# Kernel tuning notes

Measured on AMD Instinct MI355X. Metric: run time of the kernel, lower is better.

The kernel has to match this reference:

```python
import jax, jax.numpy as jnp
import numpy as np

B, S, D, H = 2, 2048, 1024, 16
DK = D // H
NEG = -1.0e9

def setup_inputs() -> dict:
    key = jax.random.key(0)
    ks = jax.random.split(key, 12)
    sc = 1.0 / np.sqrt(D)
    q = jax.random.normal(ks[0], (B, S, D), jnp.float32)
    k = jax.random.normal(ks[1], (B, S, D), jnp.float32)
    v = jax.random.normal(ks[2], (B, S, D), jnp.float32)
    # causal mask: True = masked (matches masked_fill(mask == True, -1e9))
    mask = jnp.broadcast_to(jnp.triu(jnp.ones((S, S), bool), k=1)[None, None], (B, 1, S, S))
    Wq = jax.random.normal(ks[3], (D, D), jnp.float32) * sc
    bq = jnp.zeros((D,), jnp.float32)
    Wk = jax.random.normal(ks[4], (D, D), jnp.float32) * sc
    bk = jnp.zeros((D,), jnp.float32)
    Wv = jax.random.normal(ks[5], (D, D), jnp.float32) * sc
    bv = jnp.zeros((D,), jnp.float32)
    Wo = jax.random.normal(ks[6], (D, D), jnp.float32) * sc
    bo = jnp.zeros((D,), jnp.float32)
    return {"q": q, "k": k, "v": v, "mask": mask,
            "Wq": Wq, "bq": bq, "Wk": Wk, "bk": bk,
            "Wv": Wv, "bv": bv, "Wo": Wo, "bo": bo}

def reference(q, k, v, mask, Wq, bq, Wk, bk, Wv, bv, Wo, bo):
    def split_heads(x):  # [B,S,D] -> [B,H,S,DK]
        return x.reshape(B, S, H, DK).transpose(0, 2, 1, 3)
    qh = split_heads(q @ Wq + bq)
    kh = split_heads(k @ Wk + bk)
    vh = split_heads(v @ Wv + bv)
    scores = jnp.einsum('bhqd,bhkd->bhqk', qh, kh) / np.sqrt(DK)
    scores = jnp.where(mask, NEG, scores)
    p = jax.nn.softmax(scores, axis=-1)
    out = jnp.einsum('bhqk,bhkd->bhqd', p, vh)  # [B,H,S,DK]
    out = out.transpose(0, 2, 1, 3).reshape(B, S, D)
    return out @ Wo + bo
```

## Files before the change

kernel.cpp:

```cpp
#include <hip/hip_runtime.h>

#define BB 2
#define SS 2048
#define DD 1024
#define HH 16
#define DKK 64

typedef __attribute__((ext_vector_type(8))) short short8;
typedef __attribute__((ext_vector_type(4))) float floatx4;

__device__ inline float bf2f(ushort u) {
    union { unsigned int i; float f; } x; x.i = ((unsigned int)u) << 16; return x.f;
}
__device__ inline ushort f2bf(float f) {
    union { float f; unsigned int i; } x; x.f = f;
    unsigned int r = x.i + 0x7fff + ((x.i >> 16) & 1);
    return (ushort)(r >> 16);
}
__device__ inline void async_cp16(const ushort* g, ushort* l) {
    __builtin_amdgcn_global_load_lds(
        (const __attribute__((address_space(1))) unsigned int*)g,
        (__attribute__((address_space(3))) unsigned int*)l, 16, 0, 0);
}
__device__ inline unsigned int cvt_pk_bf16(float lo, float hi) {
    unsigned int r;
    asm("v_cvt_pk_bf16_f32 %0, %1, %2" : "=v"(r) : "v"(lo), "v"(hi));
    return r;
}
__device__ inline void swap32(unsigned int& a, unsigned int& b) {
    asm("v_permlane32_swap_b32 %0, %1" : "+v"(a), "+v"(b));
}
__device__ inline void swap16(unsigned int& a, unsigned int& b) {
    asm("v_permlane16_swap_b32 %0, %1" : "+v"(a), "+v"(b));
}

__global__ __launch_bounds__(256) void cvt_w4(const float* __restrict__ w0,
                                              const float* __restrict__ w1,
                                              const float* __restrict__ w2,
                                              const float* __restrict__ w3,
                                              ushort* __restrict__ o0,
                                              ushort* __restrict__ o1,
                                              ushort* __restrict__ o2,
                                              ushort* __restrict__ o3) {
    __shared__ ushort t[32][33];
    int z = blockIdx.z;
    const float* in = (z == 0) ? w0 : (z == 1) ? w1 : (z == 2) ? w2 : w3;
    ushort* out = (z == 0) ? o0 : (z == 1) ? o1 : (z == 2) ? o2 : o3;
    int bx = blockIdx.x, by = blockIdx.y, tx = threadIdx.x;
    for (int i = threadIdx.y; i < 32; i += 8)
        t[i][tx] = f2bf(in[(size_t)(by * 32 + i) * DD + bx * 32 + tx]);
    __syncthreads();
    for (int i = threadIdx.y; i < 32; i += 8)
        out[(size_t)(bx * 32 + i) * DD + by * 32 + tx] = t[tx][i];
}

__global__ __launch_bounds__(256) void cvt_qkv(const float* __restrict__ q,
                                               const float* __restrict__ k,
                                               const float* __restrict__ v,
                                               ushort* __restrict__ oq,
                                               ushort* __restrict__ ok,
                                               ushort* __restrict__ ov) {
    int z = blockIdx.z;
    const float* in = (z == 0) ? q : (z == 1) ? k : v;
    ushort* out = (z == 0) ? oq : (z == 1) ? ok : ov;
    int i = blockIdx.x * 256 + threadIdx.x;
    float4 f0 = ((const float4*)in)[i * 2];
    float4 f1 = ((const float4*)in)[i * 2 + 1];
    short8 p;
    p[0] = (short)f2bf(f0.x); p[1] = (short)f2bf(f0.y);
    p[2] = (short)f2bf(f0.z); p[3] = (short)f2bf(f0.w);
    p[4] = (short)f2bf(f1.x); p[5] = (short)f2bf(f1.y);
    p[6] = (short)f2bf(f1.z); p[7] = (short)f2bf(f1.w);
    ((short8*)out)[i] = p;
}

__global__ __launch_bounds__(512, 2) void gemm_qkv(const ushort* __restrict__ Xq,
                                                   const ushort* __restrict__ Xk,
                                                   const ushort* __restrict__ Xv,
                                                   const ushort* __restrict__ WtQ,
                                                   const ushort* __restrict__ WtK,
                                                   const ushort* __restrict__ WtV,
                                                   const float* __restrict__ bq,
                                                   const float* __restrict__ bk,
                                                   const float* __restrict__ bv,
                                                   ushort* __restrict__ qh,
                                                   ushort* __restrict__ kh,
                                                   ushort* __restrict__ vt) {
    constexpr int K = 1024;
    constexpr int NKT = 32;
    __shared__ ushort smem[32768];

    int lin = blockIdx.x + (blockIdx.y << 2) + (blockIdx.z << 6);
    int wid = (lin & 7) * 24 + (lin >> 3);
    int z = wid >> 6;
    int rem = wid & 63;
    int byy = rem >> 2, bxx = rem & 3;
    int rowBase = byy * 256, colBase = bxx * 256;

    const ushort* Ag = (z == 0) ? Xq : (z == 1) ? Xk : Xv;
    const ushort* Bg = (z == 0) ? WtQ : (z == 1) ? WtK : WtV;
    const float* bias = (z == 0) ? bq : (z == 1) ? bk : bv;
    ushort* outp = (z == 0) ? qh : (z == 1) ? kh : vt;

    int tid = threadIdx.x;
    int wave = tid >> 6, lane = tid & 63, quad = lane >> 4, l15 = lane & 15;
    int wm = wave >> 2, wn = wave & 3;

    size_t srcA[2], srcB[2];
    int dstU[2];
#pragma unroll
    for (int r = 0; r < 2; ++r) {
        int lb = r * 8192 + wave * 1024 + lane * 16;
        int sl = lb ^ (((lb >> 9) & 1) << 5);
        int srow = sl >> 6;
        int scol = (sl & 63) >> 1;
        srcA[r] = (size_t)(rowBase + srow) * K + scol;
        srcB[r] = (size_t)(colBase + srow) * K + scol;
        dstU[r] = r * 4096 + wave * 512;
    }
    int aOff[2][4], bOff[4];
#pragma unroll
    for (int mh = 0; mh < 2; ++mh)
#pragma unroll
        for (int mi = 0; mi < 4; ++mi) {
            int row = wm * 128 + mh * 64 + mi * 16 + l15;
            aOff[mh][mi] = row * 32 + ((quad * 8) ^ (((row >> 3) & 1) << 4));
        }
#pragma unroll
    for (int ni = 0; ni < 4; ++ni) {
        int row = wn * 64 + ni * 16 + l15;
        bOff[ni] = 8192 + row * 32 + ((quad * 8) ^ (((row >> 3) & 1) << 4));
    }

    auto stageTile = [&](int u) {
        int slot = (u & 1) << 14;
        const ushort* As = Ag + u * 32;
        const ushort* Bs = Bg + u * 32;
        async_cp16(As + srcA[0], &smem[slot + dstU[0]]);
        async_cp16(As + srcA[1], &smem[slot + dstU[1]]);
        async_cp16(Bs + srcB[0], &smem[slot + 8192 + dstU[0]]);
        async_cp16(Bs + srcB[1], &smem[slot + 8192 + dstU[1]]);
    };

    floatx4 acc[8][4] = {};
    stageTile(0);
    for (int t = 0; t < NKT; ++t) {
        if (t < NKT - 1) {
            stageTile(t + 1);
            asm volatile("s_waitcnt vmcnt(4)" ::: "memory");
        } else {
            asm volatile("s_waitcnt vmcnt(0)" ::: "memory");
        }
        __builtin_amdgcn_s_barrier();
        __builtin_amdgcn_sched_barrier(0);
        int slot = (t & 1) << 14;
        short8 bfr[4];
#pragma unroll
        for (int ni = 0; ni < 4; ++ni)
            bfr[ni] = *(const short8*)&smem[slot + bOff[ni]];
#pragma unroll
        for (int mh = 0; mh < 2; ++mh) {
            short8 af[4];
#pragma unroll
            for (int mi = 0; mi < 4; ++mi)
                af[mi] = *(const short8*)&smem[slot + aOff[mh][mi]];
#pragma unroll
            for (int mi = 0; mi < 4; ++mi)
#pragma unroll
                for (int ni = 0; ni < 4; ++ni)
                    acc[mh * 4 + mi][ni] = __builtin_amdgcn_mfma_f32_16x16x32_bf16(
                        af[mi], bfr[ni], acc[mh * 4 + mi][ni], 0, 0, 0);
        }
        __builtin_amdgcn_sched_barrier(0);
        __builtin_amdgcn_s_barrier();
    }

    float bvv[4];
#pragma unroll
    for (int ni = 0; ni < 4; ++ni)
        bvv[ni] = bias[colBase + wn * 64 + ni * 16 + l15];
    if (z == 2) {
#pragma unroll
        for (int mi = 0; mi < 8; ++mi)
#pragma unroll
            for (int ni = 0; ni < 4; ++ni) {
                int col = colBase + wn * 64 + ni * 16 + l15;
                int h = col >> 6, dk = col & 63;
                int rowg = rowBase + wm * 128 + mi * 16 + quad * 4;
                int b = rowg >> 11, s = rowg & 2047;
                int2 v;
                v.x = (int)cvt_pk_bf16(acc[mi][ni][0] + bvv[ni], acc[mi][ni][1] + bvv[ni]);
                v.y = (int)cvt_pk_bf16(acc[mi][ni][2] + bvv[ni], acc[mi][ni][3] + bvv[ni]);
                *(int2*)&outp[((size_t)((b * HH + h) * DKK + dk)) * SS + s] = v;
            }
    } else {
#pragma unroll
        for (int mi = 0; mi < 8; ++mi)
#pragma unroll
            for (int ni = 0; ni < 4; ++ni) {
                int col = colBase + wn * 64 + ni * 16 + l15;
                int h = col >> 6, dk = col & 63;
#pragma unroll
                for (int i = 0; i < 4; ++i) {
                    int rowg = rowBase + wm * 128 + mi * 16 + quad * 4 + i;
                    int b = rowg >> 11, s = rowg & 2047;
                    outp[((size_t)((b * HH + h) * SS + s)) * DKK + dk] =
                        f2bf(acc[mi][ni][i] + bvv[ni]);
                }
            }
    }
}

__global__ __launch_bounds__(256) void gemm_fin(const ushort* __restrict__ A,
                                                const ushort* __restrict__ Bt,
                                                const float* __restrict__ bias,
                                                float* __restrict__ outp) {
    constexpr int K = 1024, N = 1024, NT = 32;
    __shared__ ushort smem[12288];
    int tid = threadIdx.x;
    int wave = tid >> 6, lane = tid & 63, quad = lane >> 4, l15 = lane & 15;
    int wm = wave >> 1, wn = wave & 1;

    int lin = blockIdx.x + (blockIdx.y << 3);
    int wid = (lin & 7) * 64 + (lin >> 3);
    int bx = wid & 7, by = wid >> 3;
    int rowBase = by * 64, colBase = bx * 128;

    auto stage = [&](int k0, int d) {
        int ab = d * 6144, bb2 = 2048 + d * 6144;
#pragma unroll
        for (int j = 0; j < 3; ++j) {
            int c = j * 4 + wave;
            int cbase = (c < 4) ? c * 64 : (c - 4) * 64;
            int cc = cbase + lane;
            int row = cc >> 2, sub = (cc & 3) * 8;
            if (c < 4)
                async_cp16(&A[(size_t)(rowBase + row) * K + k0 + sub], &smem[ab + cbase * 8]);
            else
                async_cp16(&Bt[(size_t)(colBase + row) * K + k0 + sub], &smem[bb2 + cbase * 8]);
        }
    };

    floatx4 acc[2][4] = {};
    stage(0, 0);
    __syncthreads();
    for (int t = 0; t < NT; ++t) {
        if (t + 1 < NT) stage((t + 1) * 32, (t + 1) & 1);
        int ab = (t & 1) * 6144, bb2 = 2048 + (t & 1) * 6144;
        short8 af[2], bf[4];
#pragma unroll
        for (int mi = 0; mi < 2; ++mi)
            af[mi] = *(const short8*)&smem[ab + (wm * 32 + mi * 16 + l15) * 32 + quad * 8];
#pragma unroll
        for (int ni = 0; ni < 4; ++ni)
            bf[ni] = *(const short8*)&smem[bb2 + (wn * 64 + ni * 16 + l15) * 32 + quad * 8];
#pragma unroll
        for (int mi = 0; mi < 2; ++mi)
#pragma unroll
            for (int ni = 0; ni < 4; ++ni)
                acc[mi][ni] = __builtin_amdgcn_mfma_f32_16x16x32_bf16(
                    af[mi], bf[ni], acc[mi][ni], 0, 0, 0);
        __syncthreads();
    }
    for (int mi = 0; mi < 2; ++mi)
        for (int ni = 0; ni < 4; ++ni) {
            int col = colBase + wn * 64 + ni * 16 + l15;
            float bv = bias[col];
            for (int i = 0; i < 4; ++i) {
                int row = rowBase + wm * 32 + mi * 16 + quad * 4 + i;
                outp[(size_t)row * N + col] = acc[mi][ni][i] + bv;
            }
        }
}

__global__ __launch_bounds__(256, 2) void flash_attn5(const ushort* __restrict__ qh,
                                                      const ushort* __restrict__ kh,
                                                      const ushort* __restrict__ vt,
                                                      ushort* __restrict__ attn) {
    constexpr int LD = 72;
    __shared__ ushort Ksm[2][64 * LD];
    __shared__ ushort Vsm[2][64 * LD];
    int tid = threadIdx.x;
    int h = blockIdx.y, b = blockIdx.z;
    int wave = tid >> 6, lane = tid & 63, quad = lane >> 4, l15 = lane & 15;
    const size_t headQK = ((size_t)(b * HH + h)) * SS * DKK;
    const size_t headV  = ((size_t)(b * HH + h)) * DKK * SS;
    int c0 = tid, r0 = c0 >> 3, s0 = (c0 & 7) * 8;
    int c1 = tid + 256, r1 = c1 >> 3, s1 = (c1 & 7) * 8;
    const int qt0 = blockIdx.x;
    const int qt1 = 31 - qt0;

    int qrow0 = qt0 * 64 + wave * 16 + l15;
    int qrow1 = qt1 * 64 + wave * 16 + l15;
    short8 q0a = *(const short8*)&qh[headQK + (size_t)qrow0 * DKK + quad * 8];
    short8 q0b = *(const short8*)&qh[headQK + (size_t)qrow0 * DKK + 32 + quad * 8];
    short8 q1a = *(const short8*)&qh[headQK + (size_t)qrow1 * DKK + quad * 8];
    short8 q1b = *(const short8*)&qh[headQK + (size_t)qrow1 * DKK + 32 + quad * 8];

    floatx4 o0[4] = {}, o1[4] = {};
    float l0 = 0.f, l1 = 0.f;
    int qsel = wave * 16 + l15;

    *(int4*)&Ksm[0][r0 * LD + s0] = *(const int4*)&kh[headQK + (size_t)r0 * DKK + s0];
    *(int4*)&Ksm[0][r1 * LD + s1] = *(const int4*)&kh[headQK + (size_t)r1 * DKK + s1];
    *(int4*)&Vsm[0][r0 * LD + s0] = *(const int4*)&vt[headV + (size_t)r0 * SS + s0];
    *(int4*)&Vsm[0][r1 * LD + s1] = *(const int4*)&vt[headV + (size_t)r1 * SS + s1];
    __syncthreads();

    for (int kt = 0; kt <= qt1; ++kt) {
        int cur = kt & 1;
        bool pre = (kt < qt1);
        bool act0 = (kt <= qt0);
        int4 kA, kB, vA, vB;
        if (pre) {
            const ushort* kp = &kh[headQK + (size_t)((kt + 1) * 64) * DKK];
            const ushort* vp = &vt[headV + (kt + 1) * 64];
            kA = *(const int4*)&kp[(size_t)r0 * DKK + s0];
            kB = *(const int4*)&kp[(size_t)r1 * DKK + s1];
            vA = *(const int4*)&vp[(size_t)r0 * SS + s0];
            vB = *(const int4*)&vp[(size_t)r1 * SS + s1];
        }
        floatx4 sv1[4], sv0[4];
#pragma unroll
        for (int cn = 0; cn < 4; ++cn) {
            short8 kf0 = *(const short8*)&Ksm[cur][(cn * 16 + l15) * LD + quad * 8];
            short8 kf1 = *(const short8*)&Ksm[cur][(cn * 16 + l15) * LD + 32 + quad * 8];
            floatx4 zz = {};
            zz = __builtin_amdgcn_mfma_f32_16x16x32_bf16(kf0, q1a, zz, 0, 0, 0);
            zz = __builtin_amdgcn_mfma_f32_16x16x32_bf16(kf1, q1b, zz, 0, 0, 0);
            sv1[cn] = zz;
            if (act0) {
                floatx4 y = {};
                y = __builtin_amdgcn_mfma_f32_16x16x32_bf16(kf0, q0a, y, 0, 0, 0);
                y = __builtin_amdgcn_mfma_f32_16x16x32_bf16(kf1, q0b, y, 0, 0, 0);
                sv0[cn] = y;
            }
        }
        short8 vf[2][4];
#pragma unroll
        for (int ks = 0; ks < 2; ++ks)
#pragma unroll
            for (int n = 0; n < 4; ++n)
                vf[ks][n] = *(const short8*)&Vsm[cur][(n * 16 + l15) * LD + ks * 32 + quad * 8];

        {
            bool diag = (kt == qt1);
            unsigned int pkd[4][2];
#pragma unroll
            for (int cn = 0; cn < 4; ++cn) {
#pragma unroll
                for (int i = 0; i < 4; ++i) {
                    float p = __expf(sv1[cn][i] * 0.125f);
                    if (diag && (cn * 16 + quad * 4 + i) > qsel) p = 0.f;
                    sv1[cn][i] = p;
                    l1 += p;
                }
                pkd[cn][0] = cvt_pk_bf16(sv1[cn][0], sv1[cn][1]);
                pkd[cn][1] = cvt_pk_bf16(sv1[cn][2], sv1[cn][3]);
            }
#pragma unroll
            for (int ks = 0; ks < 2; ++ks) {
                unsigned int a0 = pkd[ks * 2][0], b0 = pkd[ks * 2 + 1][0];
                swap32(a0, b0); swap16(a0, b0);
                unsigned int a1 = pkd[ks * 2][1], b1 = pkd[ks * 2 + 1][1];
                swap32(a1, b1); swap16(a1, b1);
                union { int4 i4; short8 s8; } u;
                u.i4 = make_int4((int)a0, (int)a1, (int)b0, (int)b1);
#pragma unroll
                for (int n = 0; n < 4; ++n)
                    o1[n] = __builtin_amdgcn_mfma_f32_16x16x32_bf16(
                        vf[ks][n], u.s8, o1[n], 0, 0, 0);
            }
        }
        if (act0) {
            bool diag = (kt == qt0);
            unsigned int pkd[4][2];
#pragma unroll
            for (int cn = 0; cn < 4; ++cn) {
#pragma unroll
                for (int i = 0; i < 4; ++i) {
                    float p = __expf(sv0[cn][i] * 0.125f);
                    if (diag && (cn * 16 + quad * 4 + i) > qsel) p = 0.f;
                    sv0[cn][i] = p;
                    l0 += p;
                }
                pkd[cn][0] = cvt_pk_bf16(sv0[cn][0], sv0[cn][1]);
                pkd[cn][1] = cvt_pk_bf16(sv0[cn][2], sv0[cn][3]);
            }
#pragma unroll
            for (int ks = 0; ks < 2; ++ks) {
                unsigned int a0 = pkd[ks * 2][0], b0 = pkd[ks * 2 + 1][0];
                swap32(a0, b0); swap16(a0, b0);
                unsigned int a1 = pkd[ks * 2][1], b1 = pkd[ks * 2 + 1][1];
                swap32(a1, b1); swap16(a1, b1);
                union { int4 i4; short8 s8; } u;
                u.i4 = make_int4((int)a0, (int)a1, (int)b0, (int)b1);
#pragma unroll
                for (int n = 0; n < 4; ++n)
                    o0[n] = __builtin_amdgcn_mfma_f32_16x16x32_bf16(
                        vf[ks][n], u.s8, o0[n], 0, 0, 0);
            }
        }
        if (pre) {
            int nb = cur ^ 1;
            *(int4*)&Ksm[nb][r0 * LD + s0] = kA;
            *(int4*)&Ksm[nb][r1 * LD + s1] = kB;
            *(int4*)&Vsm[nb][r0 * LD + s0] = vA;
            *(int4*)&Vsm[nb][r1 * LD + s1] = vB;
        }
        __syncthreads();
    }
    l0 += __shfl_xor(l0, 16, 64); l0 += __shfl_xor(l0, 32, 64);
    l1 += __shfl_xor(l1, 16, 64); l1 += __shfl_xor(l1, 32, 64);
    float inv0 = 1.0f / l0, inv1 = 1.0f / l1;
    size_t rowOff0 = ((size_t)(b * SS + qt0 * 64 + wave * 16 + l15)) * DD + h * 64;
    size_t rowOff1 = ((size_t)(b * SS + qt1 * 64 + wave * 16 + l15)) * DD + h * 64;
#pragma unroll
    for (int n = 0; n < 4; ++n) {
        int dof = n * 16 + quad * 4;
        int2 v0, v1;
        v0.x = (int)cvt_pk_bf16(o0[n][0] * inv0, o0[n][1] * inv0);
        v0.y = (int)cvt_pk_bf16(o0[n][2] * inv0, o0[n][3] * inv0);
        v1.x = (int)cvt_pk_bf16(o1[n][0] * inv1, o1[n][1] * inv1);
        v1.y = (int)cvt_pk_bf16(o1[n][2] * inv1, o1[n][3] * inv1);
        *(int2*)&attn[rowOff0 + dof] = v0;
        *(int2*)&attn[rowOff1 + dof] = v1;
    }
}

extern "C" void kernel_launch(void* const* d_in, const int* in_sizes, int n_in,
                              void* d_out, int out_size, void* d_ws, size_t ws_size,
                              hipStream_t stream) {
    const float* q  = (const float*)d_in[0];
    const float* k  = (const float*)d_in[1];
    const float* v  = (const float*)d_in[2];
    const float* Wq = (const float*)d_in[4];
    const float* bq = (const float*)d_in[5];
    const float* Wk = (const float*)d_in[6];
    const float* bk = (const float*)d_in[7];
    const float* Wv = (const float*)d_in[8];
    const float* bv = (const float*)d_in[9];
    const float* Wo = (const float*)d_in[10];
    const float* bo = (const float*)d_in[11];

    ushort* ws   = (ushort*)d_ws;
    ushort* WtQ  = ws;
    ushort* WtK  = WtQ + (1u << 20);
    ushort* WtV  = WtK + (1u << 20);
    ushort* WtO  = WtV + (1u << 20);
    ushort* Xv   = WtO + (1u << 20);
    ushort* qh   = Xv + (4u << 20);
    ushort* kh   = qh + (4u << 20);
    ushort* vt   = kh + (4u << 20);
    ushort* Xq   = (ushort*)d_out;
    ushort* Xk   = Xq + (4u << 20);
    ushort* attn = Xv;

    cvt_w4<<<dim3(32, 32, 4), dim3(32, 8), 0, stream>>>(Wq, Wk, Wv, Wo,
                                                        WtQ, WtK, WtV, WtO);
    cvt_qkv<<<dim3(2048, 1, 3), 256, 0, stream>>>(q, k, v, Xq, Xk, Xv);

    gemm_qkv<<<dim3(4, 16, 3), 512, 0, stream>>>(Xq, Xk, Xv, WtQ, WtK, WtV,
                                                 bq, bk, bv, qh, kh, vt);

    flash_attn5<<<dim3(16, 16, 2), 256, 0, stream>>>(qh, kh, vt, attn);

    gemm_fin<<<dim3(8, 64), 256, 0, stream>>>(attn, WtO, bo, (float*)d_out);
}
```

Before: 241.6 us.

## Split paired-tile attention into one q-tile per block with remapped scheduling

Replaces the paired causal q-tile scheme, where each block handled tiles qt and 31-qt sharing K/V loads, with one q-tile per block and twice as many blocks. A linear block id is remapped so that the longest tiles (largest qt) are scheduled first and blocks are interleaved across heads. Launch bounds rise to 4 blocks per CU for higher occupancy. The trade is that K/V tiles are no longer shared between two q-tiles, so each K/V tile is reloaded more often and the block workload is imbalanced, which now relies on the scheduling order.

```diff
diff --git a/kernel.cpp b/kernel.cpp
--- a/kernel.cpp
+++ b/kernel.cpp
@@ -273,7 +273,7 @@
         }
 }
 
-__global__ __launch_bounds__(256, 2) void flash_attn5(const ushort* __restrict__ qh,
+__global__ __launch_bounds__(256, 4) void flash_attn6(const ushort* __restrict__ qh,
                                                       const ushort* __restrict__ kh,
                                                       const ushort* __restrict__ vt,
                                                       ushort* __restrict__ attn) {
@@ -281,24 +281,25 @@
     __shared__ ushort Ksm[2][64 * LD];
     __shared__ ushort Vsm[2][64 * LD];
     int tid = threadIdx.x;
-    int h = blockIdx.y, b = blockIdx.z;
     int wave = tid >> 6, lane = tid & 63, quad = lane >> 4, l15 = lane & 15;
+
+    int lin = blockIdx.x + (blockIdx.y << 5) + (blockIdx.z << 9);
+    int wid = (lin & 7) * 128 + (lin >> 3);
+    int qt = 31 - (wid & 31);
+    int h = (wid >> 5) & 15;
+    int b = wid >> 9;
+
     const size_t headQK = ((size_t)(b * HH + h)) * SS * DKK;
     const size_t headV  = ((size_t)(b * HH + h)) * DKK * SS;
     int c0 = tid, r0 = c0 >> 3, s0 = (c0 & 7) * 8;
     int c1 = tid + 256, r1 = c1 >> 3, s1 = (c1 & 7) * 8;
-    const int qt0 = blockIdx.x;
-    const int qt1 = 31 - qt0;
-
-    int qrow0 = qt0 * 64 + wave * 16 + l15;
-    int qrow1 = qt1 * 64 + wave * 16 + l15;
-    short8 q0a = *(const short8*)&qh[headQK + (size_t)qrow0 * DKK + quad * 8];
-    short8 q0b = *(const short8*)&qh[headQK + (size_t)qrow0 * DKK + 32 + quad * 8];
-    short8 q1a = *(const short8*)&qh[headQK + (size_t)qrow1 * DKK + quad * 8];
-    short8 q1b = *(const short8*)&qh[headQK + (size_t)qrow1 * DKK + 32 + quad * 8];
-
-    floatx4 o0[4] = {}, o1[4] = {};
-    float l0 = 0.f, l1 = 0.f;
+
+    int qrow = qt * 64 + wave * 16 + l15;
+    short8 qa = *(const short8*)&qh[headQK + (size_t)qrow * DKK + quad * 8];
+    short8 qb = *(const short8*)&qh[headQK + (size_t)qrow * DKK + 32 + quad * 8];
+
+    floatx4 o[4] = {};
+    float l = 0.f;
     int qsel = wave * 16 + l15;
 
     *(int4*)&Ksm[0][r0 * LD + s0] = *(const int4*)&kh[headQK + (size_t)r0 * DKK + s0];
@@ -307,10 +308,9 @@
     *(int4*)&Vsm[0][r1 * LD + s1] = *(const int4*)&vt[headV + (size_t)r1 * SS + s1];
     __syncthreads();
 
-    for (int kt = 0; kt <= qt1; ++kt) {
+    for (int kt = 0; kt <= qt; ++kt) {
         int cur = kt & 1;
-        bool pre = (kt < qt1);
-        bool act0 = (kt <= qt0);
+        bool pre = (kt < qt);
         int4 kA, kB, vA, vB;
         if (pre) {
             const ushort* kp = &kh[headQK + (size_t)((kt + 1) * 64) * DKK];
@@ -320,21 +320,15 @@
             vA = *(const int4*)&vp[(size_t)r0 * SS + s0];
             vB = *(const int4*)&vp[(size_t)r1 * SS + s1];
         }
-        floatx4 sv1[4], sv0[4];
+        floatx4 sv[4];
 #pragma unroll
         for (int cn = 0; cn < 4; ++cn) {
             short8 kf0 = *(const short8*)&Ksm[cur][(cn * 16 + l15) * LD + quad * 8];
             short8 kf1 = *(const short8*)&Ksm[cur][(cn * 16 + l15) * LD + 32 + quad * 8];
-            floatx4 zz = {};
-            zz = __builtin_amdgcn_mfma_f32_16x16x32_bf16(kf0, q1a, zz, 0, 0, 0);
-            zz = __builtin_amdgcn_mfma_f32_16x16x32_bf16(kf1, q1b, zz, 0, 0, 0);
-            sv1[cn] = zz;
-            if (act0) {
-                floatx4 y = {};
-                y = __builtin_amdgcn_mfma_f32_16x16x32_bf16(kf0, q0a, y, 0, 0, 0);
-                y = __builtin_amdgcn_mfma_f32_16x16x32_bf16(kf1, q0b, y, 0, 0, 0);
-                sv0[cn] = y;
-            }
+            floatx4 z = {};
+            z = __builtin_amdgcn_mfma_f32_16x16x32_bf16(kf0, qa, z, 0, 0, 0);
+            z = __builtin_amdgcn_mfma_f32_16x16x32_bf16(kf1, qb, z, 0, 0, 0);
+            sv[cn] = z;
         }
         short8 vf[2][4];
 #pragma unroll
@@ -343,63 +337,32 @@
             for (int n = 0; n < 4; ++n)
                 vf[ks][n] = *(const short8*)&Vsm[cur][(n * 16 + l15) * LD + ks * 32 + quad * 8];
 
-        {
-            bool diag = (kt == qt1);
-            unsigned int pkd[4][2];
-#pragma unroll
-            for (int cn = 0; cn < 4; ++cn) {
-#pragma unroll
-                for (int i = 0; i < 4; ++i) {
-                    float p = __expf(sv1[cn][i] * 0.125f);
-                    if (diag && (cn * 16 + quad * 4 + i) > qsel) p = 0.f;
-                    sv1[cn][i] = p;
-                    l1 += p;
-                }
-                pkd[cn][0] = cvt_pk_bf16(sv1[cn][0], sv1[cn][1]);
-                pkd[cn][1] = cvt_pk_bf16(sv1[cn][2], sv1[cn][3]);
+        bool diag = (kt == qt);
+        unsigned int pkd[4][2];
+#pragma unroll
+        for (int cn = 0; cn < 4; ++cn) {
+#pragma unroll
+            for (int i = 0; i < 4; ++i) {
+                float p = __expf(sv[cn][i] * 0.125f);
+                if (diag && (cn * 16 + quad * 4 + i) > qsel) p = 0.f;
+                sv[cn][i] = p;
+                l += p;
             }
-#pragma unroll
-            for (int ks = 0; ks < 2; ++ks) {
-                unsigned int a0 = pkd[ks * 2][0], b0 = pkd[ks * 2 + 1][0];
-                swap32(a0, b0); swap16(a0, b0);
-                unsigned int a1 = pkd[ks * 2][1], b1 = pkd[ks * 2 + 1][1];
-                swap32(a1, b1); swap16(a1, b1);
-                union { int4 i4; short8 s8; } u;
-                u.i4 = make_int4((int)a0, (int)a1, (int)b0, (int)b1);
-#pragma unroll
-                for (int n = 0; n < 4; ++n)
-                    o1[n] = __builtin_amdgcn_mfma_f32_16x16x32_bf16(
-                        vf[ks][n], u.s8, o1[n], 0, 0, 0);
-            }
-        }
-        if (act0) {
-            bool diag = (kt == qt0);
-            unsigned int pkd[4][2];
-#pragma unroll
-            for (int cn = 0; cn < 4; ++cn) {
-#pragma unroll
-                for (int i = 0; i < 4; ++i) {
-                    float p = __expf(sv0[cn][i] * 0.125f);
-                    if (diag && (cn * 16 + quad * 4 + i) > qsel) p = 0.f;
-                    sv0[cn][i] = p;
-                    l0 += p;
-                }
-                pkd[cn][0] = cvt_pk_bf16(sv0[cn][0], sv0[cn][1]);
-                pkd[cn][1] = cvt_pk_bf16(sv0[cn][2], sv0[cn][3]);
-            }
-#pragma unroll
-            for (int ks = 0; ks < 2; ++ks) {
-                unsigned int a0 = pkd[ks * 2][0], b0 = pkd[ks * 2 + 1][0];
-                swap32(a0, b0); swap16(a0, b0);
-                unsigned int a1 = pkd[ks * 2][1], b1 = pkd[ks * 2 + 1][1];
-                swap32(a1, b1); swap16(a1, b1);
-                union { int4 i4; short8 s8; } u;
-                u.i4 = make_int4((int)a0, (int)a1, (int)b0, (int)b1);
-#pragma unroll
-                for (int n = 0; n < 4; ++n)
-                    o0[n] = __builtin_amdgcn_mfma_f32_16x16x32_bf16(
-                        vf[ks][n], u.s8, o0[n], 0, 0, 0);
-            }
+            pkd[cn][0] = cvt_pk_bf16(sv[cn][0], sv[cn][1]);
+            pkd[cn][1] = cvt_pk_bf16(sv[cn][2], sv[cn][3]);
+        }
+#pragma unroll
+        for (int ks = 0; ks < 2; ++ks) {
+            unsigned int a0 = pkd[ks * 2][0], b0 = pkd[ks * 2 + 1][0];
+            swap32(a0, b0); swap16(a0, b0);
+            unsigned int a1 = pkd[ks * 2][1], b1 = pkd[ks * 2 + 1][1];
+            swap32(a1, b1); swap16(a1, b1);
+            union { int4 i4; short8 s8; } u;
+            u.i4 = make_int4((int)a0, (int)a1, (int)b0, (int)b1);
+#pragma unroll
+            for (int n = 0; n < 4; ++n)
+                o[n] = __builtin_amdgcn_mfma_f32_16x16x32_bf16(
+                    vf[ks][n], u.s8, o[n], 0, 0, 0);
         }
         if (pre) {
             int nb = cur ^ 1;
@@ -410,21 +373,17 @@
         }
         __syncthreads();
     }
-    l0 += __shfl_xor(l0, 16, 64); l0 += __shfl_xor(l0, 32, 64);
-    l1 += __shfl_xor(l1, 16, 64); l1 += __shfl_xor(l1, 32, 64);
-    float inv0 = 1.0f / l0, inv1 = 1.0f / l1;
-    size_t rowOff0 = ((size_t)(b * SS + qt0 * 64 + wave * 16 + l15)) * DD + h * 64;
-    size_t rowOff1 = ((size_t)(b * SS + qt1 * 64 + wave * 16 + l15)) * DD + h * 64;
+    l += __shfl_xor(l, 16, 64);
+    l += __shfl_xor(l, 32, 64);
+    float inv = 1.0f / l;
+    size_t rowOff = ((size_t)(b * SS + qt * 64 + wave * 16 + l15)) * DD + h * 64;
 #pragma unroll
     for (int n = 0; n < 4; ++n) {
         int dof = n * 16 + quad * 4;
-        int2 v0, v1;
-        v0.x = (int)cvt_pk_bf16(o0[n][0] * inv0, o0[n][1] * inv0);
-        v0.y = (int)cvt_pk_bf16(o0[n][2] * inv0, o0[n][3] * inv0);
-        v1.x = (int)cvt_pk_bf16(o1[n][0] * inv1, o1[n][1] * inv1);
-        v1.y = (int)cvt_pk_bf16(o1[n][2] * inv1, o1[n][3] * inv1);
-        *(int2*)&attn[rowOff0 + dof] = v0;
-        *(int2*)&attn[rowOff1 + dof] = v1;
+        int2 v;
+        v.x = (int)cvt_pk_bf16(o[n][0] * inv, o[n][1] * inv);
+        v.y = (int)cvt_pk_bf16(o[n][2] * inv, o[n][3] * inv);
+        *(int2*)&attn[rowOff + dof] = v;
     }
 }
 
@@ -463,7 +422,7 @@
     gemm_qkv<<<dim3(4, 16, 3), 512, 0, stream>>>(Xq, Xk, Xv, WtQ, WtK, WtV,
                                                  bq, bk, bv, qh, kh, vt);
 
-    flash_attn5<<<dim3(16, 16, 2), 256, 0, stream>>>(qh, kh, vt, attn);
+    flash_attn6<<<dim3(32, 16, 2), 256, 0, stream>>>(qh, kh, vt, attn);
 
     gemm_fin<<<dim3(8, 64), 256, 0, stream>>>(attn, WtO, bo, (float*)d_out);
 }
```

After: 246.2 us. About the same (+1.9%).

## Fuse fp32-to-bf16 input conversion into QKV GEMM loads and add MFMA priority hints

Applied to the files above, without the earlier changes.

Drops the separate cvt_qkv kernel. The QKV GEMM now reads fp32 activations straight from global memory into registers, converts them to bf16, and writes them swizzled into LDS, while B tiles still use async global-to-LDS copies. This removes one kernel launch and the round trip of writing and re-reading a bf16 copy of the activations, but the A path becomes register-staged, which costs extra VGPRs and adds a vmcnt(0) wait inside the loop. The flash attention kernel also gains s_setprio around its MFMA sections to favour matrix issue across waves.

```diff
diff --git a/kernel.cpp b/kernel.cpp
--- a/kernel.cpp
+++ b/kernel.cpp
@@ -54,29 +54,9 @@
         out[(size_t)(bx * 32 + i) * DD + by * 32 + tx] = t[tx][i];
 }
 
-__global__ __launch_bounds__(256) void cvt_qkv(const float* __restrict__ q,
-                                               const float* __restrict__ k,
-                                               const float* __restrict__ v,
-                                               ushort* __restrict__ oq,
-                                               ushort* __restrict__ ok,
-                                               ushort* __restrict__ ov) {
-    int z = blockIdx.z;
-    const float* in = (z == 0) ? q : (z == 1) ? k : v;
-    ushort* out = (z == 0) ? oq : (z == 1) ? ok : ov;
-    int i = blockIdx.x * 256 + threadIdx.x;
-    float4 f0 = ((const float4*)in)[i * 2];
-    float4 f1 = ((const float4*)in)[i * 2 + 1];
-    short8 p;
-    p[0] = (short)f2bf(f0.x); p[1] = (short)f2bf(f0.y);
-    p[2] = (short)f2bf(f0.z); p[3] = (short)f2bf(f0.w);
-    p[4] = (short)f2bf(f1.x); p[5] = (short)f2bf(f1.y);
-    p[6] = (short)f2bf(f1.z); p[7] = (short)f2bf(f1.w);
-    ((short8*)out)[i] = p;
-}
-
-__global__ __launch_bounds__(512, 2) void gemm_qkv(const ushort* __restrict__ Xq,
-                                                   const ushort* __restrict__ Xk,
-                                                   const ushort* __restrict__ Xv,
+__global__ __launch_bounds__(512, 2) void gemm_qkv(const float* __restrict__ Xq,
+                                                   const float* __restrict__ Xk,
+                                                   const float* __restrict__ Xv,
                                                    const ushort* __restrict__ WtQ,
                                                    const ushort* __restrict__ WtK,
                                                    const ushort* __restrict__ WtV,
@@ -97,7 +77,7 @@
     int byy = rem >> 2, bxx = rem & 3;
     int rowBase = byy * 256, colBase = bxx * 256;
 
-    const ushort* Ag = (z == 0) ? Xq : (z == 1) ? Xk : Xv;
+    const float*  Ag = (z == 0) ? Xq : (z == 1) ? Xk : Xv;
     const ushort* Bg = (z == 0) ? WtQ : (z == 1) ? WtK : WtV;
     const float* bias = (z == 0) ? bq : (z == 1) ? bk : bv;
     ushort* outp = (z == 0) ? qh : (z == 1) ? kh : vt;
@@ -106,15 +86,18 @@
     int wave = tid >> 6, lane = tid & 63, quad = lane >> 4, l15 = lane & 15;
     int wm = wave >> 2, wn = wave & 3;
 
-    size_t srcA[2], srcB[2];
+    int rowA[2], kcolA[2], dstSwzA[2];
+    size_t srcB[2];
     int dstU[2];
 #pragma unroll
     for (int r = 0; r < 2; ++r) {
         int lb = r * 8192 + wave * 1024 + lane * 16;
         int sl = lb ^ (((lb >> 9) & 1) << 5);
+        rowA[r] = lb >> 6;
+        kcolA[r] = (lb & 63) >> 1;
+        dstSwzA[r] = sl >> 1;
         int srow = sl >> 6;
         int scol = (sl & 63) >> 1;
-        srcA[r] = (size_t)(rowBase + srow) * K + scol;
         srcB[r] = (size_t)(colBase + srow) * K + scol;
         dstU[r] = r * 4096 + wave * 512;
     }
@@ -132,27 +115,44 @@
         bOff[ni] = 8192 + row * 32 + ((quad * 8) ^ (((row >> 3) & 1) << 4));
     }
 
-    auto stageTile = [&](int u) {
+    float4 fA[4];
+    auto loadA = [&](int u) {
+#pragma unroll
+        for (int r = 0; r < 2; ++r) {
+            const float* p = Ag + (size_t)(rowBase + rowA[r]) * K + u * 32 + kcolA[r];
+            fA[r * 2]     = *(const float4*)p;
+            fA[r * 2 + 1] = *(const float4*)(p + 4);
+        }
+    };
+    auto writeA = [&](int u) {
         int slot = (u & 1) << 14;
-        const ushort* As = Ag + u * 32;
+#pragma unroll
+        for (int r = 0; r < 2; ++r) {
+            int4 w;
+            w.x = (int)cvt_pk_bf16(fA[r * 2].x,     fA[r * 2].y);
+            w.y = (int)cvt_pk_bf16(fA[r * 2].z,     fA[r * 2].w);
+            w.z = (int)cvt_pk_bf16(fA[r * 2 + 1].x, fA[r * 2 + 1].y);
+            w.w = (int)cvt_pk_bf16(fA[r * 2 + 1].z, fA[r * 2 + 1].w);
+            *(int4*)&smem[slot + dstSwzA[r]] = w;
+        }
+    };
+    auto stageB = [&](int u) {
+        int slot = (u & 1) << 14;
         const ushort* Bs = Bg + u * 32;
-        async_cp16(As + srcA[0], &smem[slot + dstU[0]]);
-        async_cp16(As + srcA[1], &smem[slot + dstU[1]]);
         async_cp16(Bs + srcB[0], &smem[slot + 8192 + dstU[0]]);
         async_cp16(Bs + srcB[1], &smem[slot + 8192 + dstU[1]]);
     };
 
     floatx4 acc[8][4] = {};
-    stageTile(0);
+    loadA(0); stageB(0);
+    asm volatile("s_waitcnt vmcnt(0)" ::: "memory");
+    writeA(0);
+    asm volatile("s_waitcnt lgkmcnt(0)" ::: "memory");
+    __builtin_amdgcn_s_barrier();
+
     for (int t = 0; t < NKT; ++t) {
-        if (t < NKT - 1) {
-            stageTile(t + 1);
-            asm volatile("s_waitcnt vmcnt(4)" ::: "memory");
-        } else {
-            asm volatile("s_waitcnt vmcnt(0)" ::: "memory");
-        }
-        __builtin_amdgcn_s_barrier();
-        __builtin_amdgcn_sched_barrier(0);
+        bool more = (t + 1 < NKT);
+        if (more) { loadA(t + 1); stageB(t + 1); }
         int slot = (t & 1) << 14;
         short8 bfr[4];
 #pragma unroll
@@ -171,7 +171,11 @@
                     acc[mh * 4 + mi][ni] = __builtin_amdgcn_mfma_f32_16x16x32_bf16(
                         af[mi], bfr[ni], acc[mh * 4 + mi][ni], 0, 0, 0);
         }
-        __builtin_amdgcn_sched_barrier(0);
+        if (more) {
+            asm volatile("s_waitcnt vmcnt(0)" ::: "memory");
+            writeA(t + 1);
+        }
+        asm volatile("s_waitcnt lgkmcnt(0)" ::: "memory");
         __builtin_amdgcn_s_barrier();
     }
 
@@ -321,6 +325,7 @@
             vB = *(const int4*)&vp[(size_t)r1 * SS + s1];
         }
         floatx4 sv1[4], sv0[4];
+        __builtin_amdgcn_s_setprio(1);
 #pragma unroll
         for (int cn = 0; cn < 4; ++cn) {
             short8 kf0 = *(const short8*)&Ksm[cur][(cn * 16 + l15) * LD + quad * 8];
@@ -336,6 +341,7 @@
                 sv0[cn] = y;
             }
         }
+        __builtin_amdgcn_s_setprio(0);
         short8 vf[2][4];
 #pragma unroll
         for (int ks = 0; ks < 2; ++ks)
@@ -358,6 +364,7 @@
                 pkd[cn][0] = cvt_pk_bf16(sv1[cn][0], sv1[cn][1]);
                 pkd[cn][1] = cvt_pk_bf16(sv1[cn][2], sv1[cn][3]);
             }
+            __builtin_amdgcn_s_setprio(1);
 #pragma unroll
             for (int ks = 0; ks < 2; ++ks) {
                 unsigned int a0 = pkd[ks * 2][0], b0 = pkd[ks * 2 + 1][0];
@@ -371,6 +378,7 @@
                     o1[n] = __builtin_amdgcn_mfma_f32_16x16x32_bf16(
                         vf[ks][n], u.s8, o1[n], 0, 0, 0);
             }
+            __builtin_amdgcn_s_setprio(0);
         }
         if (act0) {
             bool diag = (kt == qt0);
@@ -387,6 +395,7 @@
                 pkd[cn][0] = cvt_pk_bf16(sv0[cn][0], sv0[cn][1]);
                 pkd[cn][1] = cvt_pk_bf16(sv0[cn][2], sv0[cn][3]);
             }
+            __builtin_amdgcn_s_setprio(1);
 #pragma unroll
             for (int ks = 0; ks < 2; ++ks) {
                 unsigned int a0 = pkd[ks * 2][0], b0 = pkd[ks * 2 + 1][0];
@@ -400,6 +409,7 @@
                     o0[n] = __builtin_amdgcn_mfma_f32_16x16x32_bf16(
                         vf[ks][n], u.s8, o0[n], 0, 0, 0);
             }
+            __builtin_amdgcn_s_setprio(0);
         }
         if (pre) {
             int nb = cur ^ 1;
@@ -448,19 +458,15 @@
     ushort* WtK  = WtQ + (1u << 20);
     ushort* WtV  = WtK + (1u << 20);
     ushort* WtO  = WtV + (1u << 20);
-    ushort* Xv   = WtO + (1u << 20);
-    ushort* qh   = Xv + (4u << 20);
+    ushort* attn = WtO + (1u << 20);
+    ushort* qh   = attn + (4u << 20);
     ushort* kh   = qh + (4u << 20);
     ushort* vt   = kh + (4u << 20);
-    ushort* Xq   = (ushort*)d_out;
-    ushort* Xk   = Xq + (4u << 20);
-    ushort* attn = Xv;
 
     cvt_w4<<<dim3(32, 32, 4), dim3(32, 8), 0, stream>>>(Wq, Wk, Wv, Wo,
                                                         WtQ, WtK, WtV, WtO);
-    cvt_qkv<<<dim3(2048, 1, 3), 256, 0, stream>>>(q, k, v, Xq, Xk, Xv);
-
-    gemm_qkv<<<dim3(4, 16, 3), 512, 0, stream>>>(Xq, Xk, Xv, WtQ, WtK, WtV,
+
+    gemm_qkv<<<dim3(4, 16, 3), 512, 0, stream>>>(q, k, v, WtQ, WtK, WtV,
                                                  bq, bk, bv, qh, kh, vt);
 
     flash_attn5<<<dim3(16, 16, 2), 256, 0, stream>>>(qh, kh, vt, attn);
```

Result: slower. 250.6 us (+3.8%).
